# Performance work log

Hardware: AMD Instinct MI355X
Metric: run time of the kernel (lower is better)

## Reference

```python
import jax, jax.numpy as jnp
import numpy as np

NUM_ROUNDS = 3


def squash(x, axis=-1):
    # s_norm / (1 + s_norm) * x / sqrt(s_norm), matching the torch code exactly
    s_norm = jnp.sum(x * x, axis=axis, keepdims=True)
    return (s_norm / (1.0 + s_norm)) * x / jnp.sqrt(s_norm)


def setup_inputs() -> dict:
    key = jax.random.key(0)
    k1, k2 = jax.random.split(key)
    x = jax.random.normal(k1, (512, 1152, 8), dtype=jnp.float32)   # [B, R, Cin]
    W = jax.random.normal(k2, (10, 1152, 8, 16), dtype=jnp.float32)  # [N, R, Cin, Cout]
    return {"x": x, "W": W}


def reference(x, W):
    # priors = x[None,:,:,None,:] @ W[:,None,:,:,:]  -> [N, B, R, 1, Cout]
    priors = jnp.einsum('bri,nrio->nbro', x, W)[:, :, :, None, :]
    logits = jnp.zeros_like(priors)  # [N, B, R, 1, Cout]
    outps = None
    for i in range(NUM_ROUNDS):
        probs = jax.nn.softmax(logits, axis=2)  # softmax over routes R
        outps = squash(jnp.sum(probs * priors, axis=2, keepdims=True))  # [N, B, 1, 1, Cout]
        if i != NUM_ROUNDS - 1:
            # agreement logit update: dot over Cout
            logits = logits + jnp.sum(priors * outps, axis=-1, keepdims=True)
    return outps
```

## Files before the change

kernel.cpp:

```cpp
#include <hip/hip_runtime.h>
#include <math.h>

#define R_ROUTES 1152
#define CIN 8
#define COUT 16
#define BATCH 512
#define NCAPS 10
#define NUM_ROUNDS 3

typedef __fp16 h2 __attribute__((ext_vector_type(2)));
union U32H2 { unsigned int u; h2 h; };

__device__ __forceinline__ unsigned int pkrtz(float lo, float hi) {
    U32H2 v; v.h = __builtin_amdgcn_cvt_pkrtz(lo, hi);
    return v.u;
}
__device__ __forceinline__ h2 as_h2(unsigned int u) { U32H2 v; v.u = u; return v.h; }
__device__ __forceinline__ float f_lo(unsigned int u) { return (float)as_h2(u).x; }
__device__ __forceinline__ float f_hi(unsigned int u) { return (float)as_h2(u).y; }
__device__ __forceinline__ float dot2(unsigned int p, unsigned int s, float c) {
    return __builtin_amdgcn_fdot2(as_h2(p), as_h2(s), c, false);
}

__device__ __forceinline__ int sunit(int r, int h) {
    return (2 * r + h) ^ ((r >> 2) & 7);
}

extern "C" __global__ void __launch_bounds__(256)
pack_w(const float* __restrict__ W, unsigned int* __restrict__ Wp)
{
    const int tau = blockIdx.x * 256 + threadIdx.x;
    const int o = tau & 15;
    const int nr = tau >> 4;
    const float* __restrict__ src = W + (size_t)nr * 128 + o;
    uint4 u;
    u.x = pkrtz(src[0],  src[16]);
    u.y = pkrtz(src[32], src[48]);
    u.z = pkrtz(src[64], src[80]);
    u.w = pkrtz(src[96], src[112]);
    *(uint4*)(Wp + (size_t)tau * 4) = u;
}

extern "C" __global__ void __launch_bounds__(512, 4)
capsule_routing_v9(const float* __restrict__ x,
                   const unsigned int* __restrict__ Wp,
                   float* __restrict__ out)
{
    __shared__ unsigned int pbuf[2 * R_ROUTES * 8];
    __shared__ float wred[16 * 16];
    __shared__ float red[2 * 32 * 20];
    __shared__ float sred[2 * 4];
    __shared__ float sv[2 * 16];

    const int blk = blockIdx.x;
    const int n = blk >> 8;
    const int bp = blk & 255;
    const int t = threadIdx.x;

    const float* __restrict__ x0 = x + (size_t)(2 * bp) * (R_ROUTES * CIN);
    const float* __restrict__ x1 = x0 + R_ROUTES * CIN;
    const unsigned int* __restrict__ Wn = Wp + (size_t)n * (R_ROUTES * 64);

    float cs[2][4] = {{0.f, 0.f, 0.f, 0.f}, {0.f, 0.f, 0.f, 0.f}};
    {
        const int q = t >> 2;
        const int oq = t & 3;
        const int subw = (oq & 1) * 2;
        const int hq = oq >> 1;

        #pragma unroll 1
        for (int it = 0; it < 9; ++it) {
            const int r = it * 128 + q;
            const unsigned int* __restrict__ wb = Wn + (size_t)r * 64;
            const uint4 w0 = *(const uint4*)(wb + (oq + 0) * 4);
            const uint4 w1 = *(const uint4*)(wb + (oq + 4) * 4);
            const uint4 w2 = *(const uint4*)(wb + (oq + 8) * 4);
            const uint4 w3 = *(const uint4*)(wb + (oq + 12) * 4);
            const float4 xa0 = *(const float4*)(x0 + r * 8);
            const float4 xa1 = *(const float4*)(x0 + r * 8 + 4);
            const float4 xb0 = *(const float4*)(x1 + r * 8);
            const float4 xb1 = *(const float4*)(x1 + r * 8 + 4);

            {
                const unsigned int xp0 = pkrtz(xa0.x, xa0.y), xp1 = pkrtz(xa0.z, xa0.w);
                const unsigned int xp2 = pkrtz(xa1.x, xa1.y), xp3 = pkrtz(xa1.z, xa1.w);
                const float p0 = dot2(w0.w, xp3, dot2(w0.z, xp2, dot2(w0.y, xp1, dot2(w0.x, xp0, 0.f))));
                const float p1 = dot2(w1.w, xp3, dot2(w1.z, xp2, dot2(w1.y, xp1, dot2(w1.x, xp0, 0.f))));
                const float p2 = dot2(w2.w, xp3, dot2(w2.z, xp2, dot2(w2.y, xp1, dot2(w2.x, xp0, 0.f))));
                const float p3 = dot2(w3.w, xp3, dot2(w3.z, xp2, dot2(w3.y, xp1, dot2(w3.x, xp0, 0.f))));
                cs[0][0] += p0; cs[0][1] += p1; cs[0][2] += p2; cs[0][3] += p3;
                uint2 u; u.x = pkrtz(p0, p1); u.y = pkrtz(p2, p3);
                *(uint2*)(pbuf + sunit(r, hq) * 4 + subw) = u;
            }
            {
                const unsigned int xp0 = pkrtz(xb0.x, xb0.y), xp1 = pkrtz(xb0.z, xb0.w);
                const unsigned int xp2 = pkrtz(xb1.x, xb1.y), xp3 = pkrtz(xb1.z, xb1.w);
                const float p0 = dot2(w0.w, xp3, dot2(w0.z, xp2, dot2(w0.y, xp1, dot2(w0.x, xp0, 0.f))));
                const float p1 = dot2(w1.w, xp3, dot2(w1.z, xp2, dot2(w1.y, xp1, dot2(w1.x, xp0, 0.f))));
                const float p2 = dot2(w2.w, xp3, dot2(w2.z, xp2, dot2(w2.y, xp1, dot2(w2.x, xp0, 0.f))));
                const float p3 = dot2(w3.w, xp3, dot2(w3.z, xp2, dot2(w3.y, xp1, dot2(w3.x, xp0, 0.f))));
                cs[1][0] += p0; cs[1][1] += p1; cs[1][2] += p2; cs[1][3] += p3;
                uint2 u; u.x = pkrtz(p0, p1); u.y = pkrtz(p2, p3);
                *(uint2*)(pbuf + R_ROUTES * 8 + sunit(r, hq) * 4 + subw) = u;
            }
        }

        #pragma unroll
        for (int mask = 4; mask <= 32; mask <<= 1) {
            #pragma unroll
            for (int b = 0; b < 2; ++b)
                #pragma unroll
                for (int j = 0; j < 4; ++j)
                    cs[b][j] += __shfl_xor(cs[b][j], mask, 64);
        }
        if ((t & 63) < 4) {
            const int w = t >> 6;
            *(float4*)(wred + (w * 2 + 0) * 16 + 4 * oq) =
                make_float4(cs[0][0], cs[0][1], cs[0][2], cs[0][3]);
            *(float4*)(wred + (w * 2 + 1) * 16 + 4 * oq) =
                make_float4(cs[1][0], cs[1][1], cs[1][2], cs[1][3]);
        }
    }
    __syncthreads();

    const int half = t >> 8;
    const int tt = t & 255;
    unsigned int* __restrict__ pb = pbuf + half * (R_ROUTES * 8);
    float* __restrict__ redh = red + half * (32 * 20);
    float* __restrict__ sredh = sred + half * 4;
    float* __restrict__ svh = sv + half * 16;

    if (tt < 16) {
        float s = 0.f;
        #pragma unroll
        for (int w = 0; w < 8; ++w) s += wred[(w * 2 + half) * 16 + tt];
        svh[tt] = s * (1.0f / (float)R_ROUTES);
    }
    __syncthreads();

    float sn = 0.f;
    #pragma unroll
    for (int o = 0; o < 16; ++o) { const float s = svh[o]; sn = fmaf(s, s, sn); }
    float factor = sn / ((1.0f + sn) * sqrtf(sn));

    const int nr = (tt < 128) ? 5 : 4;
    float bl[5] = {0.f, 0.f, 0.f, 0.f, 0.f};

    #pragma unroll 1
    for (int pass = 1; pass < NUM_ROUNDS; ++pass) {
        unsigned int svp[8];
        #pragma unroll
        for (int s = 0; s < 8; ++s)
            svp[s] = pkrtz(svh[2 * s], svh[2 * s + 1]);
        float acc[16];
        #pragma unroll
        for (int o = 0; o < 16; ++o) acc[o] = 0.f;
        float es = 0.f;

        #pragma unroll
        for (int k = 0; k < 5; ++k) {
            if (k < nr) {
                const int r = tt + (k << 8);
                const uint4 a = *(const uint4*)(pb + sunit(r, 0) * 4);
                const uint4 c = *(const uint4*)(pb + sunit(r, 1) * 4);
                float d = 0.f;
                d = dot2(a.x, svp[0], d);
                d = dot2(a.y, svp[1], d);
                d = dot2(a.z, svp[2], d);
                d = dot2(a.w, svp[3], d);
                d = dot2(c.x, svp[4], d);
                d = dot2(c.y, svp[5], d);
                d = dot2(c.z, svp[6], d);
                d = dot2(c.w, svp[7], d);
                bl[k] = fmaf(factor, d, bl[k]);
                const float e = __expf(bl[k]);
                es += e;
                acc[0]  = fmaf(e, f_lo(a.x), acc[0]);
                acc[1]  = fmaf(e, f_hi(a.x), acc[1]);
                acc[2]  = fmaf(e, f_lo(a.y), acc[2]);
                acc[3]  = fmaf(e, f_hi(a.y), acc[3]);
                acc[4]  = fmaf(e, f_lo(a.z), acc[4]);
                acc[5]  = fmaf(e, f_hi(a.z), acc[5]);
                acc[6]  = fmaf(e, f_lo(a.w), acc[6]);
                acc[7]  = fmaf(e, f_hi(a.w), acc[7]);
                acc[8]  = fmaf(e, f_lo(c.x), acc[8]);
                acc[9]  = fmaf(e, f_hi(c.x), acc[9]);
                acc[10] = fmaf(e, f_lo(c.y), acc[10]);
                acc[11] = fmaf(e, f_hi(c.y), acc[11]);
                acc[12] = fmaf(e, f_lo(c.z), acc[12]);
                acc[13] = fmaf(e, f_hi(c.z), acc[13]);
                acc[14] = fmaf(e, f_lo(c.w), acc[14]);
                acc[15] = fmaf(e, f_hi(c.w), acc[15]);
            }
        }
        #pragma unroll
        for (int off = 32; off > 0; off >>= 1) es += __shfl_xor(es, off, 64);
        if ((t & 63) == 0) sredh[tt >> 6] = es;

        #pragma unroll
        for (int o = 0; o < 16; ++o) {
            acc[o] += __shfl_xor(acc[o], 1, 64);
            acc[o] += __shfl_xor(acc[o], 2, 64);
            acc[o] += __shfl_xor(acc[o], 4, 64);
        }
        if ((tt & 7) == 0) {
            float* dst = redh + (tt >> 3) * 20;
            *(float4*)(dst + 0)  = make_float4(acc[0],  acc[1],  acc[2],  acc[3]);
            *(float4*)(dst + 4)  = make_float4(acc[4],  acc[5],  acc[6],  acc[7]);
            *(float4*)(dst + 8)  = make_float4(acc[8],  acc[9],  acc[10], acc[11]);
            *(float4*)(dst + 12) = make_float4(acc[12], acc[13], acc[14], acc[15]);
        }
        __syncthreads();

        if (tt < 16) {
            float s = 0.f;
            #pragma unroll
            for (int w = 0; w < 32; ++w) s += redh[w * 20 + tt];
            const float Z = sredh[0] + sredh[1] + sredh[2] + sredh[3];
            svh[tt] = s / Z;
        }
        __syncthreads();

        sn = 0.f;
        #pragma unroll
        for (int o = 0; o < 16; ++o) { const float s = svh[o]; sn = fmaf(s, s, sn); }
        factor = sn / ((1.0f + sn) * sqrtf(sn));
    }

    if (tt < 16) {
        const int o = (tt >> 2) + ((tt & 3) << 2);
        out[((size_t)n * BATCH + 2 * bp + half) * COUT + o] = factor * svh[tt];
    }
}

extern "C" void kernel_launch(void* const* d_in, const int* in_sizes, int n_in,
                              void* d_out, int out_size, void* d_ws, size_t ws_size,
                              hipStream_t stream) {
    const float* x = (const float*)d_in[0];
    const float* W = (const float*)d_in[1];
    float* out = (float*)d_out;
    unsigned int* Wp = (unsigned int*)d_ws;

    pack_w<<<dim3(NCAPS * R_ROUTES * COUT / 256), dim3(256), 0, stream>>>(W, Wp);
    capsule_routing_v9<<<dim3(NCAPS * (BATCH / 2)), dim3(512), 0, stream>>>(x, Wp, out);
}
```

Before: 137.2 us.

## Pre-pack x to fp16, software-pipeline prior loads, use DPP/permlane reductions

Extends the packing kernel so it also converts x to packed fp16 in workspace. The main kernel then reads half as many bytes of x per block, and x is re-read by all ten capsule blocks. The prior-computation loop is double-buffered so the next iteration's loads overlap the current compute. Wave reductions swap __shfl_xor for DPP and permlane swap instructions, and the cross-wave final sums are spread over 64 threads. The costs are an extra pass over x in the pack kernel and a dependence on workspace size, with a fallback path when the workspace is too small.

```diff
diff --git a/kernel.cpp b/kernel.cpp
--- a/kernel.cpp
+++ b/kernel.cpp
@@ -22,43 +22,97 @@
     return __builtin_amdgcn_fdot2(as_h2(p), as_h2(s), c, false);
 }
 
+#define DPP_XOR1 0xB1
+#define DPP_XOR2 0x4E
+#define DPP_ROR4 0x124
+#define DPP_ROR8 0x128
+template<int CTRL>
+__device__ __forceinline__ float dpp_add(float v) {
+    int d = __builtin_amdgcn_update_dpp(0, __float_as_int(v), CTRL, 0xf, 0xf, false);
+    return v + __int_as_float(d);
+}
+__device__ __forceinline__ float p16_add(float v) {
+    float a = v, b = v;
+    asm("v_permlane16_swap_b32 %0, %1" : "+v"(a), "+v"(b));
+    return a + b;
+}
+__device__ __forceinline__ float p32_add(float v) {
+    float a = v, b = v;
+    asm("v_permlane32_swap_b32 %0, %1" : "+v"(a), "+v"(b));
+    return a + b;
+}
+__device__ __forceinline__ float wave_sum64(float v) {
+    v = dpp_add<DPP_XOR1>(v);
+    v = dpp_add<DPP_XOR2>(v);
+    v = dpp_add<DPP_ROR4>(v);
+    v = dpp_add<DPP_ROR8>(v);
+    v = p16_add(v);
+    return p32_add(v);
+}
+
 __device__ __forceinline__ int sunit(int r, int h) {
     return (2 * r + h) ^ ((r >> 2) & 7);
 }
 
+__device__ __forceinline__ float sq16(float4 a, float4 b, float4 c, float4 d) {
+    float sn = a.x * a.x;
+    sn = fmaf(a.y, a.y, sn); sn = fmaf(a.z, a.z, sn); sn = fmaf(a.w, a.w, sn);
+    sn = fmaf(b.x, b.x, sn); sn = fmaf(b.y, b.y, sn); sn = fmaf(b.z, b.z, sn);
+    sn = fmaf(b.w, b.w, sn);
+    sn = fmaf(c.x, c.x, sn); sn = fmaf(c.y, c.y, sn); sn = fmaf(c.z, c.z, sn);
+    sn = fmaf(c.w, c.w, sn);
+    sn = fmaf(d.x, d.x, sn); sn = fmaf(d.y, d.y, sn); sn = fmaf(d.z, d.z, sn);
+    sn = fmaf(d.w, d.w, sn);
+    return sn;
+}
+
 extern "C" __global__ void __launch_bounds__(256)
-pack_w(const float* __restrict__ W, unsigned int* __restrict__ Wp)
+pack_wx(const float* __restrict__ W, const float* __restrict__ x,
+        unsigned int* __restrict__ Wp, uint4* __restrict__ Xp)
 {
-    const int tau = blockIdx.x * 256 + threadIdx.x;
-    const int o = tau & 15;
-    const int nr = tau >> 4;
-    const float* __restrict__ src = W + (size_t)nr * 128 + o;
-    uint4 u;
-    u.x = pkrtz(src[0],  src[16]);
-    u.y = pkrtz(src[32], src[48]);
-    u.z = pkrtz(src[64], src[80]);
-    u.w = pkrtz(src[96], src[112]);
-    *(uint4*)(Wp + (size_t)tau * 4) = u;
-}
-
-extern "C" __global__ void __launch_bounds__(512, 4)
-capsule_routing_v9(const float* __restrict__ x,
-                   const unsigned int* __restrict__ Wp,
-                   float* __restrict__ out)
+    const int blk = blockIdx.x;
+    if (blk < 720) {
+        const int tau = blk * 256 + threadIdx.x;
+        const int o = tau & 15;
+        const int nr = tau >> 4;
+        const float* __restrict__ src = W + (size_t)nr * 128 + o;
+        uint4 u;
+        u.x = pkrtz(src[0],  src[16]);
+        u.y = pkrtz(src[32], src[48]);
+        u.z = pkrtz(src[64], src[80]);
+        u.w = pkrtz(src[96], src[112]);
+        *(uint4*)(Wp + (size_t)tau * 4) = u;
+    } else {
+        const int idx = (blk - 720) * 256 + threadIdx.x;
+        const float4 a = *(const float4*)(x + (size_t)idx * 8);
+        const float4 b = *(const float4*)(x + (size_t)idx * 8 + 4);
+        uint4 u;
+        u.x = pkrtz(a.x, a.y);
+        u.y = pkrtz(a.z, a.w);
+        u.z = pkrtz(b.x, b.y);
+        u.w = pkrtz(b.z, b.w);
+        Xp[idx] = u;
+    }
+}
+
+template<bool XP>
+__global__ void __launch_bounds__(512, 4)
+capsule_routing_v10(const float* __restrict__ x,
+                    const unsigned int* __restrict__ Wp,
+                    const uint4* __restrict__ Xp,
+                    float* __restrict__ out)
 {
-    __shared__ unsigned int pbuf[2 * R_ROUTES * 8];
-    __shared__ float wred[16 * 16];
-    __shared__ float red[2 * 32 * 20];
+    __shared__ __align__(16) unsigned int pbuf[2 * R_ROUTES * 8];
+    __shared__ __align__(16) float wred[16 * 16];
+    __shared__ __align__(16) float red[2 * 32 * 20];
     __shared__ float sred[2 * 4];
-    __shared__ float sv[2 * 16];
+    __shared__ __align__(16) float sv[2 * 16];
 
     const int blk = blockIdx.x;
     const int n = blk >> 8;
     const int bp = blk & 255;
     const int t = threadIdx.x;
 
-    const float* __restrict__ x0 = x + (size_t)(2 * bp) * (R_ROUTES * CIN);
-    const float* __restrict__ x1 = x0 + R_ROUTES * CIN;
     const unsigned int* __restrict__ Wn = Wp + (size_t)n * (R_ROUTES * 64);
 
     float cs[2][4] = {{0.f, 0.f, 0.f, 0.f}, {0.f, 0.f, 0.f, 0.f}};
@@ -68,51 +122,94 @@
         const int subw = (oq & 1) * 2;
         const int hq = oq >> 1;
 
-        #pragma unroll 1
-        for (int it = 0; it < 9; ++it) {
+        const float* __restrict__ x0 = x + (size_t)(2 * bp) * (R_ROUTES * CIN);
+        const float* __restrict__ x1 = x0 + R_ROUTES * CIN;
+        const uint4* __restrict__ xq0 = Xp + (size_t)(2 * bp) * R_ROUTES;
+        const uint4* __restrict__ xq1 = xq0 + R_ROUTES;
+
+        uint4 wA0, wA1, wA2, wA3, wB0, wB1, wB2, wB3;
+        uint4 xA0, xA1, xB0, xB1;
+        float4 gA0, gA1, gA2, gA3, gB0, gB1, gB2, gB3;
+
+        auto loadW = [&](int it, uint4& a0, uint4& a1, uint4& a2, uint4& a3) {
+            const unsigned int* wb = Wn + (size_t)(it * 128 + q) * 64 + oq * 4;
+            a0 = *(const uint4*)(wb + 0);
+            a1 = *(const uint4*)(wb + 16);
+            a2 = *(const uint4*)(wb + 32);
+            a3 = *(const uint4*)(wb + 48);
+        };
+        auto loadX = [&](int it, uint4& a, uint4& b,
+                         float4& g0, float4& g1, float4& g2, float4& g3) {
             const int r = it * 128 + q;
-            const unsigned int* __restrict__ wb = Wn + (size_t)r * 64;
-            const uint4 w0 = *(const uint4*)(wb + (oq + 0) * 4);
-            const uint4 w1 = *(const uint4*)(wb + (oq + 4) * 4);
-            const uint4 w2 = *(const uint4*)(wb + (oq + 8) * 4);
-            const uint4 w3 = *(const uint4*)(wb + (oq + 12) * 4);
-            const float4 xa0 = *(const float4*)(x0 + r * 8);
-            const float4 xa1 = *(const float4*)(x0 + r * 8 + 4);
-            const float4 xb0 = *(const float4*)(x1 + r * 8);
-            const float4 xb1 = *(const float4*)(x1 + r * 8 + 4);
-
+            if constexpr (XP) {
+                a = xq0[r];
+                b = xq1[r];
+            } else {
+                g0 = *(const float4*)(x0 + r * 8);
+                g1 = *(const float4*)(x0 + r * 8 + 4);
+                g2 = *(const float4*)(x1 + r * 8);
+                g3 = *(const float4*)(x1 + r * 8 + 4);
+            }
+        };
+        auto packX = [&](uint4& a, uint4& b,
+                         float4 g0, float4 g1, float4 g2, float4 g3) {
+            if constexpr (!XP) {
+                a.x = pkrtz(g0.x, g0.y); a.y = pkrtz(g0.z, g0.w);
+                a.z = pkrtz(g1.x, g1.y); a.w = pkrtz(g1.z, g1.w);
+                b.x = pkrtz(g2.x, g2.y); b.y = pkrtz(g2.z, g2.w);
+                b.z = pkrtz(g3.x, g3.y); b.w = pkrtz(g3.z, g3.w);
+            }
+        };
+        auto compute = [&](int it, uint4 w0, uint4 w1, uint4 w2, uint4 w3,
+                           uint4 xa, uint4 xb) {
+            const int r = it * 128 + q;
             {
-                const unsigned int xp0 = pkrtz(xa0.x, xa0.y), xp1 = pkrtz(xa0.z, xa0.w);
-                const unsigned int xp2 = pkrtz(xa1.x, xa1.y), xp3 = pkrtz(xa1.z, xa1.w);
-                const float p0 = dot2(w0.w, xp3, dot2(w0.z, xp2, dot2(w0.y, xp1, dot2(w0.x, xp0, 0.f))));
-                const float p1 = dot2(w1.w, xp3, dot2(w1.z, xp2, dot2(w1.y, xp1, dot2(w1.x, xp0, 0.f))));
-                const float p2 = dot2(w2.w, xp3, dot2(w2.z, xp2, dot2(w2.y, xp1, dot2(w2.x, xp0, 0.f))));
-                const float p3 = dot2(w3.w, xp3, dot2(w3.z, xp2, dot2(w3.y, xp1, dot2(w3.x, xp0, 0.f))));
+                const float p0 = dot2(w0.w, xa.w, dot2(w0.z, xa.z, dot2(w0.y, xa.y, dot2(w0.x, xa.x, 0.f))));
+                const float p1 = dot2(w1.w, xa.w, dot2(w1.z, xa.z, dot2(w1.y, xa.y, dot2(w1.x, xa.x, 0.f))));
+                const float p2 = dot2(w2.w, xa.w, dot2(w2.z, xa.z, dot2(w2.y, xa.y, dot2(w2.x, xa.x, 0.f))));
+                const float p3 = dot2(w3.w, xa.w, dot2(w3.z, xa.z, dot2(w3.y, xa.y, dot2(w3.x, xa.x, 0.f))));
                 cs[0][0] += p0; cs[0][1] += p1; cs[0][2] += p2; cs[0][3] += p3;
                 uint2 u; u.x = pkrtz(p0, p1); u.y = pkrtz(p2, p3);
                 *(uint2*)(pbuf + sunit(r, hq) * 4 + subw) = u;
             }
             {
-                const unsigned int xp0 = pkrtz(xb0.x, xb0.y), xp1 = pkrtz(xb0.z, xb0.w);
-                const unsigned int xp2 = pkrtz(xb1.x, xb1.y), xp3 = pkrtz(xb1.z, xb1.w);
-                const float p0 = dot2(w0.w, xp3, dot2(w0.z, xp2, dot2(w0.y, xp1, dot2(w0.x, xp0, 0.f))));
-                const float p1 = dot2(w1.w, xp3, dot2(w1.z, xp2, dot2(w1.y, xp1, dot2(w1.x, xp0, 0.f))));
-                const float p2 = dot2(w2.w, xp3, dot2(w2.z, xp2, dot2(w2.y, xp1, dot2(w2.x, xp0, 0.f))));
-                const float p3 = dot2(w3.w, xp3, dot2(w3.z, xp2, dot2(w3.y, xp1, dot2(w3.x, xp0, 0.f))));
+                const float p0 = dot2(w0.w, xb.w, dot2(w0.z, xb.z, dot2(w0.y, xb.y, dot2(w0.x, xb.x, 0.f))));
+                const float p1 = dot2(w1.w, xb.w, dot2(w1.z, xb.z, dot2(w1.y, xb.y, dot2(w1.x, xb.x, 0.f))));
+                const float p2 = dot2(w2.w, xb.w, dot2(w2.z, xb.z, dot2(w2.y, xb.y, dot2(w2.x, xb.x, 0.f))));
+                const float p3 = dot2(w3.w, xb.w, dot2(w3.z, xb.z, dot2(w3.y, xb.y, dot2(w3.x, xb.x, 0.f))));
                 cs[1][0] += p0; cs[1][1] += p1; cs[1][2] += p2; cs[1][3] += p3;
                 uint2 u; u.x = pkrtz(p0, p1); u.y = pkrtz(p2, p3);
                 *(uint2*)(pbuf + R_ROUTES * 8 + sunit(r, hq) * 4 + subw) = u;
             }
-        }
+        };
+
+        loadW(0, wA0, wA1, wA2, wA3);
+        loadX(0, xA0, xA1, gA0, gA1, gA2, gA3);
+        #pragma unroll 1
+        for (int it = 0; it < 8; it += 2) {
+            loadW(it + 1, wB0, wB1, wB2, wB3);
+            loadX(it + 1, xB0, xB1, gB0, gB1, gB2, gB3);
+            packX(xA0, xA1, gA0, gA1, gA2, gA3);
+            compute(it, wA0, wA1, wA2, wA3, xA0, xA1);
+            loadW(it + 2, wA0, wA1, wA2, wA3);
+            loadX(it + 2, xA0, xA1, gA0, gA1, gA2, gA3);
+            packX(xB0, xB1, gB0, gB1, gB2, gB3);
+            compute(it + 1, wB0, wB1, wB2, wB3, xB0, xB1);
+        }
+        packX(xA0, xA1, gA0, gA1, gA2, gA3);
+        compute(8, wA0, wA1, wA2, wA3, xA0, xA1);
 
         #pragma unroll
-        for (int mask = 4; mask <= 32; mask <<= 1) {
+        for (int b = 0; b < 2; ++b)
             #pragma unroll
-            for (int b = 0; b < 2; ++b)
-                #pragma unroll
-                for (int j = 0; j < 4; ++j)
-                    cs[b][j] += __shfl_xor(cs[b][j], mask, 64);
-        }
+            for (int j = 0; j < 4; ++j) {
+                float v = cs[b][j];
+                v = dpp_add<DPP_ROR4>(v);
+                v = dpp_add<DPP_ROR8>(v);
+                v = p16_add(v);
+                v = p32_add(v);
+                cs[b][j] = v;
+            }
         if ((t & 63) < 4) {
             const int w = t >> 6;
             *(float4*)(wred + (w * 2 + 0) * 16 + 4 * oq) =
@@ -130,17 +227,20 @@
     float* __restrict__ sredh = sred + half * 4;
     float* __restrict__ svh = sv + half * 16;
 
-    if (tt < 16) {
-        float s = 0.f;
-        #pragma unroll
-        for (int w = 0; w < 8; ++w) s += wred[(w * 2 + half) * 16 + tt];
-        svh[tt] = s * (1.0f / (float)R_ROUTES);
+    if (tt < 64) {
+        const int k = tt & 15, wg = tt >> 4;
+        float s = wred[(wg * 2 + half) * 16 + k] + wred[((wg + 4) * 2 + half) * 16 + k];
+        s = p16_add(s);
+        s = p32_add(s);
+        if (tt < 16) svh[tt] = s * (1.0f / (float)R_ROUTES);
     }
     __syncthreads();
 
-    float sn = 0.f;
-    #pragma unroll
-    for (int o = 0; o < 16; ++o) { const float s = svh[o]; sn = fmaf(s, s, sn); }
+    float4 s0 = *(const float4*)(svh + 0);
+    float4 s1 = *(const float4*)(svh + 4);
+    float4 s2 = *(const float4*)(svh + 8);
+    float4 s3 = *(const float4*)(svh + 12);
+    float sn = sq16(s0, s1, s2, s3);
     float factor = sn / ((1.0f + sn) * sqrtf(sn));
 
     const int nr = (tt < 128) ? 5 : 4;
@@ -149,9 +249,10 @@
     #pragma unroll 1
     for (int pass = 1; pass < NUM_ROUNDS; ++pass) {
         unsigned int svp[8];
-        #pragma unroll
-        for (int s = 0; s < 8; ++s)
-            svp[s] = pkrtz(svh[2 * s], svh[2 * s + 1]);
+        svp[0] = pkrtz(s0.x, s0.y); svp[1] = pkrtz(s0.z, s0.w);
+        svp[2] = pkrtz(s1.x, s1.y); svp[3] = pkrtz(s1.z, s1.w);
+        svp[4] = pkrtz(s2.x, s2.y); svp[5] = pkrtz(s2.z, s2.w);
+        svp[6] = pkrtz(s3.x, s3.y); svp[7] = pkrtz(s3.z, s3.w);
         float acc[16];
         #pragma unroll
         for (int o = 0; o < 16; ++o) acc[o] = 0.f;
@@ -193,15 +294,16 @@
                 acc[15] = fmaf(e, f_hi(c.w), acc[15]);
             }
         }
-        #pragma unroll
-        for (int off = 32; off > 0; off >>= 1) es += __shfl_xor(es, off, 64);
+        es = wave_sum64(es);
         if ((t & 63) == 0) sredh[tt >> 6] = es;
 
         #pragma unroll
         for (int o = 0; o < 16; ++o) {
-            acc[o] += __shfl_xor(acc[o], 1, 64);
-            acc[o] += __shfl_xor(acc[o], 2, 64);
-            acc[o] += __shfl_xor(acc[o], 4, 64);
+            float v = acc[o];
+            v = dpp_add<DPP_XOR1>(v);
+            v = dpp_add<DPP_XOR2>(v);
+            v = dpp_add<DPP_ROR4>(v);
+            acc[o] = v;
         }
         if ((tt & 7) == 0) {
             float* dst = redh + (tt >> 3) * 20;
@@ -212,18 +314,25 @@
         }
         __syncthreads();
 
-        if (tt < 16) {
+        if (tt < 64) {
+            const int k = tt & 15, wg = tt >> 4;
             float s = 0.f;
             #pragma unroll
-            for (int w = 0; w < 32; ++w) s += redh[w * 20 + tt];
-            const float Z = sredh[0] + sredh[1] + sredh[2] + sredh[3];
-            svh[tt] = s / Z;
+            for (int i = 0; i < 8; ++i) s += redh[(wg * 8 + i) * 20 + k];
+            s = p16_add(s);
+            s = p32_add(s);
+            if (tt < 16) {
+                const float Z = sredh[0] + sredh[1] + sredh[2] + sredh[3];
+                svh[tt] = s / Z;
+            }
         }
         __syncthreads();
 
-        sn = 0.f;
-        #pragma unroll
-        for (int o = 0; o < 16; ++o) { const float s = svh[o]; sn = fmaf(s, s, sn); }
+        s0 = *(const float4*)(svh + 0);
+        s1 = *(const float4*)(svh + 4);
+        s2 = *(const float4*)(svh + 8);
+        s3 = *(const float4*)(svh + 12);
+        sn = sq16(s0, s1, s2, s3);
         factor = sn / ((1.0f + sn) * sqrtf(sn));
     }
 
@@ -239,8 +348,17 @@
     const float* x = (const float*)d_in[0];
     const float* W = (const float*)d_in[1];
     float* out = (float*)d_out;
+
     unsigned int* Wp = (unsigned int*)d_ws;
-
-    pack_w<<<dim3(NCAPS * R_ROUTES * COUT / 256), dim3(256), 0, stream>>>(W, Wp);
-    capsule_routing_v9<<<dim3(NCAPS * (BATCH / 2)), dim3(512), 0, stream>>>(x, Wp, out);
-}
+    const size_t WPB = (size_t)NCAPS * R_ROUTES * COUT * 16;
+    const size_t XPB = (size_t)BATCH * R_ROUTES * 16;
+    uint4* Xp = (uint4*)((char*)d_ws + WPB);
+
+    if (ws_size >= WPB + XPB) {
+        pack_wx<<<dim3(720 + 2304), dim3(256), 0, stream>>>(W, x, Wp, Xp);
+        capsule_routing_v10<true><<<dim3(NCAPS * (BATCH / 2)), dim3(512), 0, stream>>>(x, Wp, Xp, out);
+    } else {
+        pack_wx<<<dim3(720), dim3(256), 0, stream>>>(W, x, Wp, Xp);
+        capsule_routing_v10<false><<<dim3(NCAPS * (BATCH / 2)), dim3(512), 0, stream>>>(x, Wp, Xp, out);
+    }
+}
```

Result: faster. 129.8 us (-5.4%).
